# Kernel tuning notes

Hardware: AMD Instinct MI355X
Metric: run time of the kernel (lower is better)

Reference implementation:

```python
import jax, jax.numpy as jnp
import numpy as np

FH = FW = 3          # field_height, field_width
SF = 2               # scale_factor passed to set_transforms
NODES = 32           # out_channels
D_IN = 16            # in_channels (field depth)
HID = 32             # mlpnodes[0]; mlpnodes = [32, 1]


def maxpool_3x3_s2_p1(x):
    # Deterministic stand-in for FractionalMaxPool2d(kernel=3, output=(H//2, W//2)):
    return jax.lax.reduce_window(
        x, -jnp.inf, jax.lax.max,
        window_dimensions=(1, 1, 3, 3),
        window_strides=(1, 1, 2, 2),
        padding=((0, 0), (0, 0), (1, 1), (1, 1)))


def unfold_3x3(x):
    # torch.nn.Unfold(kernel=(3,3), padding=1): (N,D,H,W) -> (N, D, 9, H*W)
    N, D, H, W = x.shape
    xp = jnp.pad(x, ((0, 0), (0, 0), (1, 1), (1, 1)))
    patches = jnp.stack([xp[:, :, i:i + H, j:j + W]
                         for i in range(3) for j in range(3)], axis=2)
    return patches.reshape(N, D, 9, H * W)


def setup_inputs() -> dict:
    key = jax.random.key(0)
    k = jax.random.split(key, 6)
    N, H, W = 32, 96, 96
    x = jax.random.normal(k[0], (N, D_IN, H, W), dtype=jnp.float32)
    # S per node: xavier_uniform on shape (1, D, 3, 3): fan_in=D*9, fan_out=1*9
    bound_S = float(np.sqrt(6.0 / (D_IN * 9 + 9)))
    S = jax.random.uniform(k[1], (NODES, D_IN, FH, FW), jnp.float32, -bound_S, bound_S)
    # per-node MLP: Linear(D_IN -> HID) -> ReLU -> Linear(HID -> 1) -> ReLU
    b1w = 1.0 / np.sqrt(D_IN)
    W1 = jax.random.uniform(k[2], (NODES, D_IN, HID), jnp.float32, -b1w, b1w)
    b1 = jax.random.uniform(k[3], (NODES, HID), jnp.float32, -b1w, b1w)
    b2w = 1.0 / np.sqrt(HID)
    W2 = jax.random.uniform(k[4], (NODES, HID, 1), jnp.float32, -b2w, b2w)
    b2 = jax.random.uniform(k[5], (NODES, 1), jnp.float32, -b2w, b2w)
    return {"x": x, "S": S, "W1": W1, "b1": b1, "W2": W2, "b2": b2}


def reference(x, S, W1, b1, W2, b2):
    N, D, H, W = x.shape
    Hs, Ws = H // SF, W // SF
    U = unfold_3x3(maxpool_3x3_s2_p1(x))            # (N, D, 9, L), L = Hs*Ws
    Sf = S.reshape(S.shape[0], D, FH * FW)          # (O, D, 9)
    # StructFun: M[n,d,l] = sum_k S[d,k] * U[n,d,k,l], batched over nodes o
    M = jnp.einsum('odk,ndkl->nlod', Sf, U)         # (N, L, O, D)
    # StructBlock: reshape to (N,Hs,Ws,D) then per-node MLP over last dim
    h = jax.nn.relu(jnp.einsum('nlod,odh->nloh', M, W1) + b1)   # (N, L, O, HID)
    y = jax.nn.relu(jnp.einsum('nloh,ohe->nloe', h, W2) + b2)   # (N, L, O, 1)
    out = y[..., 0].reshape(N, Hs, Ws, -1)          # (N, Hs, Ws, O)
    return out.transpose(0, 3, 1, 2)                # (N, O, Hs, Ws)
```

## Files before the change

### kernel.cpp

```cpp
#include <hip/hip_runtime.h>
#include <math.h>

typedef __bf16 bf16;
typedef __bf16 bf16x8 __attribute__((ext_vector_type(8)));
typedef float  f32x16 __attribute__((ext_vector_type(16)));

#define D_INC 16
#define NODES 32
#define HID   32
#define HS    48
#define WSZ   48
#define NPX   (HS*WSZ)
#define H_IN  96
#define W_IN  96
#define N_B   32

#define MP_BLOCKS   1152
#define WPRE_BLOCKS 640

__global__ __launch_bounds__(256) void pre_kernel(
    const float* __restrict__ x, bf16* __restrict__ Pg,
    const float* __restrict__ S, const float* __restrict__ W1,
    const float* __restrict__ b1, bf16* __restrict__ Wp)
{
    if (blockIdx.x < MP_BLOCKS) {
        int idx = blockIdx.x * 256 + threadIdx.x;
        int q = idx & 3;
        int c = (idx >> 2) % WSZ;
        int t = (idx >> 2) / WSZ;
        int r = t % HS;
        int n = t / HS;

        const float* xb = x + ((size_t)(n * D_INC + q * 4)) * (H_IN * W_IN);

        float m0 = -INFINITY, m1 = -INFINITY, m2 = -INFINITY, m3 = -INFINITY;
        #pragma unroll
        for (int dr = 0; dr < 3; ++dr) {
            int xr = 2 * r - 1 + dr;
            if (xr < 0) continue;
            #pragma unroll
            for (int dc = 0; dc < 3; ++dc) {
                int xc = 2 * c - 1 + dc;
                if (xc < 0) continue;
                const float* p = xb + xr * W_IN + xc;
                m0 = fmaxf(m0, p[0 * H_IN * W_IN]);
                m1 = fmaxf(m1, p[1 * H_IN * W_IN]);
                m2 = fmaxf(m2, p[2 * H_IN * W_IN]);
                m3 = fmaxf(m3, p[3 * H_IN * W_IN]);
            }
        }
        union { bf16 h[4]; uint2 u; } v;
        v.h[0] = (bf16)m0; v.h[1] = (bf16)m1; v.h[2] = (bf16)m2; v.h[3] = (bf16)m3;
        *(uint2*)(Pg + (size_t)idx * 4) = v.u;
    } else {
        int idx = (blockIdx.x - MP_BLOCKS) * 256 + threadIdx.x;
        if (idx >= NODES * 10 * 2 * HID * 8) return;
        int j  = idx & 7;
        int h  = (idx >> 3) & 31;
        int qp = (idx >> 8) & 1;
        int os = idx >> 9;
        int s  = os % 10;
        int o  = os / 10;
        int k  = 16 * s + 8 * qp + j;
        float v = 0.f;
        if (k < 144) {
            int t = k >> 4;
            int d = k & 15;
            v = S[(o * D_INC + d) * 9 + t] * W1[(o * D_INC + d) * HID + h];
        } else if (k == 144) {
            v = b1[o * HID + h];
        }
        Wp[idx] = (bf16)v;
    }
}

__global__ __launch_bounds__(256, 2) void gemm_kernel(
    const bf16* __restrict__ Pg, const bf16* __restrict__ Wp,
    const float* __restrict__ W2, const float* __restrict__ b2,
    float* __restrict__ out)
{
    __shared__ __align__(16) bf16  Pl[8 * 50 * D_INC];
    __shared__ __align__(16) float W2l[4 * HID];

    const int b    = blockIdx.x;
    const int n    = blockIdx.y;
    const int ob   = blockIdx.z * 4;
    const int tid  = threadIdx.x;
    const int lane = tid & 63;
    const int w    = tid >> 6;
    const int ln31 = lane & 31;
    const int qp   = lane >> 5;

    const int px0     = b * 256;
    const int r_start = px0 / 48;

    const uint4 z4 = make_uint4(0u, 0u, 0u, 0u);

    for (int u = tid; u < 768; u += 256) {
        int half = u & 1;
        int colu = (u >> 1) % 48;
        int row  = (u >> 1) / 48;
        int pr   = r_start - 1 + row;
        uint4 v  = z4;
        if (pr >= 0 && pr < HS)
            v = *(const uint4*)(Pg + ((size_t)(n * HS + pr) * WSZ + colu) * D_INC + half * 8);
        *(uint4*)(Pl + (row * 50 + colu + 1) * D_INC + half * 8) = v;
    }
    if (tid < 32) {
        int row  = tid >> 2;
        int side = (tid >> 1) & 1;
        int half = tid & 1;
        *(uint4*)(Pl + (row * 50 + side * 49) * D_INC + half * 8) = z4;
    }
    if (tid < 32)
        ((float4*)W2l)[tid] = ((const float4*)(W2 + ob * HID))[tid];
    __syncthreads();

    int base_ad[2];
    int pxg[2];
    #pragma unroll
    for (int t = 0; t < 2; ++t) {
        int px = px0 + w * 64 + t * 32 + ln31;
        int r  = px / 48;
        int c  = px - r * 48;
        int rl = r - r_start;
        base_ad[t] = ((rl * 50) + c) * 32 + qp * 16;
        pxg[t] = px;
    }

    bf16x8 Bf[2][10];
    #pragma unroll
    for (int t = 0; t < 2; ++t) {
        #pragma unroll
        for (int s = 0; s < 9; ++s) {
            const int di = s / 3, dj = s % 3;
            Bf[t][s] = *(const bf16x8*)((const char*)Pl + base_ad[t] + (di * 50 + dj) * 32);
        }
        bf16x8 bias = {};
        if (qp == 0) bias[0] = (bf16)1.0f;
        Bf[t][9] = bias;
    }

    for (int o4 = 0; o4 < 4; ++o4) {
        const int o = ob + o4;

        const bf16* wp = Wp + (size_t)(o * 10) * 512 + lane * 8;
        bf16x8 Af[10];
        #pragma unroll
        for (int s = 0; s < 10; ++s)
            Af[s] = *(const bf16x8*)(wp + s * 512);

        const float* w2b = W2l + o4 * HID + 4 * qp;
        float4 w2v0 = *(const float4*)(w2b);
        float4 w2v1 = *(const float4*)(w2b + 8);
        float4 w2v2 = *(const float4*)(w2b + 16);
        float4 w2v3 = *(const float4*)(w2b + 24);
        const float bb = b2[o];

        f32x16 acc0 = {};
        f32x16 acc1 = {};
        #pragma unroll
        for (int s = 0; s < 10; ++s) {
            acc0 = __builtin_amdgcn_mfma_f32_32x32x16_bf16(Af[s], Bf[0][s], acc0, 0, 0, 0);
            acc1 = __builtin_amdgcn_mfma_f32_32x32x16_bf16(Af[s], Bf[1][s], acc1, 0, 0, 0);
        }

        #pragma unroll
        for (int t = 0; t < 2; ++t) {
            const f32x16 a = t ? acc1 : acc0;
            float part;
            part  = fmaxf(a[0],  0.f) * w2v0.x;
            part  = fmaf(fmaxf(a[1],  0.f), w2v0.y, part);
            part  = fmaf(fmaxf(a[2],  0.f), w2v0.z, part);
            part  = fmaf(fmaxf(a[3],  0.f), w2v0.w, part);
            part  = fmaf(fmaxf(a[4],  0.f), w2v1.x, part);
            part  = fmaf(fmaxf(a[5],  0.f), w2v1.y, part);
            part  = fmaf(fmaxf(a[6],  0.f), w2v1.z, part);
            part  = fmaf(fmaxf(a[7],  0.f), w2v1.w, part);
            part  = fmaf(fmaxf(a[8],  0.f), w2v2.x, part);
            part  = fmaf(fmaxf(a[9],  0.f), w2v2.y, part);
            part  = fmaf(fmaxf(a[10], 0.f), w2v2.z, part);
            part  = fmaf(fmaxf(a[11], 0.f), w2v2.w, part);
            part  = fmaf(fmaxf(a[12], 0.f), w2v3.x, part);
            part  = fmaf(fmaxf(a[13], 0.f), w2v3.y, part);
            part  = fmaf(fmaxf(a[14], 0.f), w2v3.z, part);
            part  = fmaf(fmaxf(a[15], 0.f), w2v3.w, part);
            float tot = part + __shfl_xor(part, 32);
            tot = fmaxf(tot + bb, 0.f);
            if (qp == 0)
                out[(size_t)(n * NODES + o) * NPX + pxg[t]] = tot;
        }
    }
}

extern "C" void kernel_launch(void* const* d_in, const int* in_sizes, int n_in,
                              void* d_out, int out_size, void* d_ws, size_t ws_size,
                              hipStream_t stream)
{
    const float* x  = (const float*)d_in[0];
    const float* S  = (const float*)d_in[1];
    const float* W1 = (const float*)d_in[2];
    const float* b1 = (const float*)d_in[3];
    const float* W2 = (const float*)d_in[4];
    const float* b2 = (const float*)d_in[5];
    float* out = (float*)d_out;

    bf16* Pg = (bf16*)d_ws;
    bf16* Wp = (bf16*)((char*)d_ws + (size_t)N_B * NPX * D_INC * 2);

    pre_kernel<<<MP_BLOCKS + WPRE_BLOCKS, 256, 0, stream>>>(x, Pg, S, W1, b1, Wp);

    dim3 grid(9, N_B, 8);
    gemm_kernel<<<grid, 256, 0, stream>>>(Pg, Wp, W2, b2, out);
}
```

Baseline: 107.9 us.

## Split gemm block work across eight waves with one pixel tile each

Doubles the gemm block size to 512 threads so each wave handles a single 32-pixel tile with one accumulator instead of two. This lowers register pressure per wave and raises resident wave count to hide latency. In exchange, each wave reloads the weight fragments for half as many pixels, and the MFMA chain per wave loses its two-way independent interleaving.

```diff
diff --git a/kernel.cpp b/kernel.cpp
--- a/kernel.cpp
+++ b/kernel.cpp
@@ -74,7 +74,7 @@
     }
 }
 
-__global__ __launch_bounds__(256, 2) void gemm_kernel(
+__global__ __launch_bounds__(512, 4) void gemm_kernel(
     const bf16* __restrict__ Pg, const bf16* __restrict__ Wp,
     const float* __restrict__ W2, const float* __restrict__ b2,
     float* __restrict__ out)
@@ -96,7 +96,7 @@
 
     const uint4 z4 = make_uint4(0u, 0u, 0u, 0u);
 
-    for (int u = tid; u < 768; u += 256) {
+    for (int u = tid; u < 768; u += 512) {
         int half = u & 1;
         int colu = (u >> 1) % 48;
         int row  = (u >> 1) / 48;
@@ -111,34 +111,26 @@
         int side = (tid >> 1) & 1;
         int half = tid & 1;
         *(uint4*)(Pl + (row * 50 + side * 49) * D_INC + half * 8) = z4;
-    }
-    if (tid < 32)
         ((float4*)W2l)[tid] = ((const float4*)(W2 + ob * HID))[tid];
+    }
     __syncthreads();
 
-    int base_ad[2];
-    int pxg[2];
+    const int px = px0 + w * 32 + ln31;
+    const int r  = px / 48;
+    const int c  = px - r * 48;
+    const int rl = r - r_start;
+    const int base_ad = ((rl * 50) + c) * 32 + qp * 16;
+
+    bf16x8 Bf[10];
     #pragma unroll
-    for (int t = 0; t < 2; ++t) {
-        int px = px0 + w * 64 + t * 32 + ln31;
-        int r  = px / 48;
-        int c  = px - r * 48;
-        int rl = r - r_start;
-        base_ad[t] = ((rl * 50) + c) * 32 + qp * 16;
-        pxg[t] = px;
-    }
-
-    bf16x8 Bf[2][10];
-    #pragma unroll
-    for (int t = 0; t < 2; ++t) {
-        #pragma unroll
-        for (int s = 0; s < 9; ++s) {
-            const int di = s / 3, dj = s % 3;
-            Bf[t][s] = *(const bf16x8*)((const char*)Pl + base_ad[t] + (di * 50 + dj) * 32);
-        }
+    for (int s = 0; s < 9; ++s) {
+        const int di = s / 3, dj = s % 3;
+        Bf[s] = *(const bf16x8*)((const char*)Pl + base_ad + (di * 50 + dj) * 32);
+    }
+    {
         bf16x8 bias = {};
         if (qp == 0) bias[0] = (bf16)1.0f;
-        Bf[t][9] = bias;
+        Bf[9] = bias;
     }
 
     for (int o4 = 0; o4 < 4; ++o4) {
@@ -149,6 +141,11 @@
         #pragma unroll
         for (int s = 0; s < 10; ++s)
             Af[s] = *(const bf16x8*)(wp + s * 512);
+
+        f32x16 acc = {};
+        #pragma unroll
+        for (int s = 0; s < 10; ++s)
+            acc = __builtin_amdgcn_mfma_f32_32x32x16_bf16(Af[s], Bf[s], acc, 0, 0, 0);
 
         const float* w2b = W2l + o4 * HID + 4 * qp;
         float4 w2v0 = *(const float4*)(w2b);
@@ -157,39 +154,27 @@
         float4 w2v3 = *(const float4*)(w2b + 24);
         const float bb = b2[o];
 
-        f32x16 acc0 = {};
-        f32x16 acc1 = {};
-        #pragma unroll
-        for (int s = 0; s < 10; ++s) {
-            acc0 = __builtin_amdgcn_mfma_f32_32x32x16_bf16(Af[s], Bf[0][s], acc0, 0, 0, 0);
-            acc1 = __builtin_amdgcn_mfma_f32_32x32x16_bf16(Af[s], Bf[1][s], acc1, 0, 0, 0);
-        }
-
-        #pragma unroll
-        for (int t = 0; t < 2; ++t) {
-            const f32x16 a = t ? acc1 : acc0;
-            float part;
-            part  = fmaxf(a[0],  0.f) * w2v0.x;
-            part  = fmaf(fmaxf(a[1],  0.f), w2v0.y, part);
-            part  = fmaf(fmaxf(a[2],  0.f), w2v0.z, part);
-            part  = fmaf(fmaxf(a[3],  0.f), w2v0.w, part);
-            part  = fmaf(fmaxf(a[4],  0.f), w2v1.x, part);
-            part  = fmaf(fmaxf(a[5],  0.f), w2v1.y, part);
-            part  = fmaf(fmaxf(a[6],  0.f), w2v1.z, part);
-            part  = fmaf(fmaxf(a[7],  0.f), w2v1.w, part);
-            part  = fmaf(fmaxf(a[8],  0.f), w2v2.x, part);
-            part  = fmaf(fmaxf(a[9],  0.f), w2v2.y, part);
-            part  = fmaf(fmaxf(a[10], 0.f), w2v2.z, part);
-            part  = fmaf(fmaxf(a[11], 0.f), w2v2.w, part);
-            part  = fmaf(fmaxf(a[12], 0.f), w2v3.x, part);
-            part  = fmaf(fmaxf(a[13], 0.f), w2v3.y, part);
-            part  = fmaf(fmaxf(a[14], 0.f), w2v3.z, part);
-            part  = fmaf(fmaxf(a[15], 0.f), w2v3.w, part);
-            float tot = part + __shfl_xor(part, 32);
-            tot = fmaxf(tot + bb, 0.f);
-            if (qp == 0)
-                out[(size_t)(n * NODES + o) * NPX + pxg[t]] = tot;
-        }
+        float part;
+        part  = fmaxf(acc[0],  0.f) * w2v0.x;
+        part  = fmaf(fmaxf(acc[1],  0.f), w2v0.y, part);
+        part  = fmaf(fmaxf(acc[2],  0.f), w2v0.z, part);
+        part  = fmaf(fmaxf(acc[3],  0.f), w2v0.w, part);
+        part  = fmaf(fmaxf(acc[4],  0.f), w2v1.x, part);
+        part  = fmaf(fmaxf(acc[5],  0.f), w2v1.y, part);
+        part  = fmaf(fmaxf(acc[6],  0.f), w2v1.z, part);
+        part  = fmaf(fmaxf(acc[7],  0.f), w2v1.w, part);
+        part  = fmaf(fmaxf(acc[8],  0.f), w2v2.x, part);
+        part  = fmaf(fmaxf(acc[9],  0.f), w2v2.y, part);
+        part  = fmaf(fmaxf(acc[10], 0.f), w2v2.z, part);
+        part  = fmaf(fmaxf(acc[11], 0.f), w2v2.w, part);
+        part  = fmaf(fmaxf(acc[12], 0.f), w2v3.x, part);
+        part  = fmaf(fmaxf(acc[13], 0.f), w2v3.y, part);
+        part  = fmaf(fmaxf(acc[14], 0.f), w2v3.z, part);
+        part  = fmaf(fmaxf(acc[15], 0.f), w2v3.w, part);
+        float tot = part + __shfl_xor(part, 32);
+        tot = fmaxf(tot + bb, 0.f);
+        if (qp == 0)
+            out[(size_t)(n * NODES + o) * NPX + px] = tot;
     }
 }
 
@@ -211,5 +196,5 @@
     pre_kernel<<<MP_BLOCKS + WPRE_BLOCKS, 256, 0, stream>>>(x, Pg, S, W1, b1, Wp);
 
     dim3 grid(9, N_B, 8);
-    gemm_kernel<<<grid, 256, 0, stream>>>(Pg, Wp, W2, b2, out);
+    gemm_kernel<<<grid, 512, 0, stream>>>(Pg, Wp, W2, b2, out);
 }
```

After: 111.4 us. +3.3%, slower.
